# Optimization experiments

Measured on AMD Instinct MI355X. Metric: run time of the kernel, lower is better.

The kernel has to match this reference:

```python
import jax, jax.numpy as jnp
import numpy as np
import math

B, T, C = 4, 2048, 1024
H = 16
D_FF = 4 * C


def new_gelu(x):
    # tanh-approx GELU, identical to the torch.jit.script version
    return 0.5 * x * (1.0 + jnp.tanh(math.sqrt(2.0 / math.pi) * (x + 0.044715 * x ** 3)))


def layernorm(x, g, b, eps=1e-5):
    mu = jnp.mean(x, axis=-1, keepdims=True)
    var = jnp.var(x, axis=-1, keepdims=True)
    return (x - mu) * jax.lax.rsqrt(var + eps) * g + b


def setup_inputs() -> dict:
    key = jax.random.key(0)
    ks = jax.random.split(key, 8)
    s = 0.02
    return {
        "x": jax.random.normal(ks[0], (B, T, C), dtype=jnp.float32),
        "ln1_g": jnp.ones((C,), jnp.float32),
        "ln1_b": jnp.zeros((C,), jnp.float32),
        "w_qkv": jax.random.normal(ks[1], (C, 3 * C), jnp.float32) * s,
        "b_qkv": jnp.zeros((3 * C,), jnp.float32),
        "w_attnproj": jax.random.normal(ks[2], (C, C), jnp.float32) * s,
        "b_attnproj": jnp.zeros((C,), jnp.float32),
        "ln2_g": jnp.ones((C,), jnp.float32),
        "ln2_b": jnp.zeros((C,), jnp.float32),
        "w_fc": jax.random.normal(ks[3], (C, D_FF), jnp.float32) * s,
        "b_fc": jnp.zeros((D_FF,), jnp.float32),
        "w_proj": jax.random.normal(ks[4], (D_FF, C), jnp.float32) * s,
        "b_proj": jnp.zeros((C,), jnp.float32),
    }


def _block(x, ln1_g, ln1_b, w_qkv, b_qkv, w_attnproj, b_attnproj,
           ln2_g, ln2_b, w_fc, b_fc, w_proj, b_proj):
    # --- self-attention (pre-LN, non-causal, dropout=0) ---
    h = layernorm(x, ln1_g, ln1_b)
    qkv = h @ w_qkv + b_qkv                       # [B,T,3C]
    q, k, v = jnp.split(qkv, 3, axis=-1)
    hd = C // H
    q = q.reshape(B, T, H, hd).transpose(0, 2, 1, 3)  # [B,H,T,hd]
    k = k.reshape(B, T, H, hd).transpose(0, 2, 1, 3)
    v = v.reshape(B, T, H, hd).transpose(0, 2, 1, 3)
    att = jnp.einsum('bhqd,bhkd->bhqk', q, k) * (1.0 / math.sqrt(hd))
    att = jax.nn.softmax(att, axis=-1)
    y = jnp.einsum('bhqk,bhkd->bhqd', att, v)
    y = y.transpose(0, 2, 1, 3).reshape(B, T, C)
    x = x + (y @ w_attnproj + b_attnproj)
    # --- MLP ---
    h = layernorm(x, ln2_g, ln2_b)
    h = new_gelu(h @ w_fc + b_fc)
    x = x + (h @ w_proj + b_proj)
    return x


def reference(x, ln1_g, ln1_b, w_qkv, b_qkv, w_attnproj, b_attnproj,
              ln2_g, ln2_b, w_fc, b_fc, w_proj, b_proj):
    return _block(x, ln1_g, ln1_b, w_qkv, b_qkv, w_attnproj, b_attnproj,
                  ln2_g, ln2_b, w_fc, b_fc, w_proj, b_proj)
```

## Files before the change

kernel.cpp:

```cpp
#include <hip/hip_runtime.h>


typedef __attribute__((ext_vector_type(8))) short short8;
typedef __attribute__((ext_vector_type(4))) float fx4;
typedef __attribute__((ext_vector_type(16))) float fx16;

__device__ __forceinline__ unsigned short f2bf(float f) {
    union { float f; unsigned u; } v; v.f = f;
    unsigned r = v.u + 0x7fffu + ((v.u >> 16) & 1u);
    return (unsigned short)(r >> 16);
}

__device__ __forceinline__ float fexp2(float x) {
#if __has_builtin(__builtin_amdgcn_exp2f)
    return __builtin_amdgcn_exp2f(x);
#else
    return __expf(x * 0.69314718055994531f);
#endif
}

__device__ __forceinline__ unsigned pack_trunc(float lo, float hi) {
    return __builtin_amdgcn_perm(__float_as_uint(hi), __float_as_uint(lo),
                                 0x07060302u);
}

__device__ __forceinline__ void ld_lds16(const void* g, void* l) {
    __builtin_amdgcn_global_load_lds(
        (const __attribute__((address_space(1))) unsigned int*)g,
        (__attribute__((address_space(3))) unsigned int*)l, 16, 0, 0);
}

__global__ __launch_bounds__(256) void transpose_all(
    const float* __restrict__ w0, unsigned short* __restrict__ o0,
    const float* __restrict__ w1, unsigned short* __restrict__ o1,
    const float* __restrict__ w2, unsigned short* __restrict__ o2,
    const float* __restrict__ w3, unsigned short* __restrict__ o3)
{
    __shared__ float tile[32][33];
    int b = blockIdx.x;
    const float* in; unsigned short* out; int R, Cn;
    if (b < 3072)      { in = w0; out = o0; R = 1024; Cn = 3072; }
    else if (b < 4096) { b -= 3072; in = w1; out = o1; R = 1024; Cn = 1024; }
    else if (b < 8192) { b -= 4096; in = w2; out = o2; R = 1024; Cn = 4096; }
    else               { b -= 8192; in = w3; out = o3; R = 4096; Cn = 1024; }
    int tilesX = Cn >> 5;
    int c0 = (b % tilesX) * 32, r0 = (b / tilesX) * 32;
    int tx = threadIdx.x, ty = threadIdx.y;
    for (int i = 0; i < 4; ++i)
        tile[ty + i * 8][tx] = in[(size_t)(r0 + ty + i * 8) * Cn + c0 + tx];
    __syncthreads();
    for (int i = 0; i < 4; ++i)
        out[(size_t)(c0 + ty + i * 8) * R + r0 + tx] = f2bf(tile[tx][ty + i * 8]);
}

__global__ __launch_bounds__(256) void layernorm_bf16(
    const float* __restrict__ x, const float* __restrict__ g,
    const float* __restrict__ bb, unsigned short* __restrict__ out)
{
    const int C = 1024;
    int row = blockIdx.x;
    const float* xr = x + (size_t)row * C;
    float4 v = ((const float4*)xr)[threadIdx.x];
    float s  = v.x + v.y + v.z + v.w;
    float ss = v.x * v.x + v.y * v.y + v.z * v.z + v.w * v.w;
    for (int off = 32; off >= 1; off >>= 1) {
        s  += __shfl_xor(s,  off);
        ss += __shfl_xor(ss, off);
    }
    __shared__ float sbuf[2][4];
    int wave = threadIdx.x >> 6;
    if ((threadIdx.x & 63) == 0) { sbuf[0][wave] = s; sbuf[1][wave] = ss; }
    __syncthreads();
    s  = sbuf[0][0] + sbuf[0][1] + sbuf[0][2] + sbuf[0][3];
    ss = sbuf[1][0] + sbuf[1][1] + sbuf[1][2] + sbuf[1][3];
    float mu   = s * (1.0f / C);
    float var  = ss * (1.0f / C) - mu * mu;
    float rstd = rsqrtf(var + 1e-5f);
    int i = threadIdx.x * 4;
    ushort4 o;
    o.x = f2bf((v.x - mu) * rstd * g[i + 0] + bb[i + 0]);
    o.y = f2bf((v.y - mu) * rstd * g[i + 1] + bb[i + 1]);
    o.z = f2bf((v.z - mu) * rstd * g[i + 2] + bb[i + 2]);
    o.w = f2bf((v.w - mu) * rstd * g[i + 3] + bb[i + 3]);
    ((ushort4*)(out + (size_t)row * C))[threadIdx.x] = o;
}

template <int EPI>
__global__ __launch_bounds__(256) void gemm_bt(
    const unsigned short* __restrict__ A, const unsigned short* __restrict__ Bt,
    const float* __restrict__ bias, const float* __restrict__ resid,
    void* __restrict__ out0, void* __restrict__ out1, void* __restrict__ out2,
    int M, int N, int K)
{
    __shared__ unsigned short As[128 * 64];
    __shared__ unsigned short Bs[128 * 64];
    const int bm = blockIdx.y * 128, bn = blockIdx.x * 128;
    const int t = threadIdx.x, wave = t >> 6, lane = t & 63;
    const int wm = (wave >> 1) * 64, wn = (wave & 1) * 64;
    const int l32 = lane & 31, half = lane >> 5;

    int goff[4], loff[4];
    #pragma unroll
    for (int c = 0; c < 4; ++c) {
        int idx = t + c * 256;
        int row = idx >> 3, ps = idx & 7;
        int p = (ps - row) & 7;
        goff[c] = row * K + p * 8;
        loff[c] = idx * 8;
    }
    int aoffs[2][4], boffs[2][4];
    #pragma unroll
    for (int i = 0; i < 2; ++i)
        #pragma unroll
        for (int s = 0; s < 4; ++s) {
            int ra = wm + i * 32 + l32;
            int rb = wn + i * 32 + l32;
            aoffs[i][s] = ra * 64 + (((s * 2 + half + ra) & 7) << 3);
            boffs[i][s] = rb * 64 + (((s * 2 + half + rb) & 7) << 3);
        }

    const unsigned short* Ab = A + (size_t)bm * K;
    const unsigned short* Bb = Bt + (size_t)bn * K;

    fx16 acc[2][2];
    #pragma unroll
    for (int mi = 0; mi < 2; ++mi)
        #pragma unroll
        for (int ni = 0; ni < 2; ++ni)
            acc[mi][ni] = 0.0f;

    for (int it = 0, nit = K >> 6; it < nit; ++it) {
        #pragma unroll
        for (int c = 0; c < 4; ++c) {
            ld_lds16(Ab + goff[c], &As[loff[c]]);
            ld_lds16(Bb + goff[c], &Bs[loff[c]]);
        }
        Ab += 64; Bb += 64;
        __syncthreads();
        #pragma unroll
        for (int s = 0; s < 4; ++s) {
            short8 a0 = *(const short8*)&As[aoffs[0][s]];
            short8 a1 = *(const short8*)&As[aoffs[1][s]];
            short8 b0 = *(const short8*)&Bs[boffs[0][s]];
            short8 b1 = *(const short8*)&Bs[boffs[1][s]];
            acc[0][0] = __builtin_amdgcn_mfma_f32_32x32x16_bf16(a0, b0, acc[0][0], 0, 0, 0);
            acc[0][1] = __builtin_amdgcn_mfma_f32_32x32x16_bf16(a0, b1, acc[0][1], 0, 0, 0);
            acc[1][0] = __builtin_amdgcn_mfma_f32_32x32x16_bf16(a1, b0, acc[1][0], 0, 0, 0);
            acc[1][1] = __builtin_amdgcn_mfma_f32_32x32x16_bf16(a1, b1, acc[1][1], 0, 0, 0);
        }
        __syncthreads();
    }

    #pragma unroll
    for (int mi = 0; mi < 2; ++mi) {
        #pragma unroll
        for (int ni = 0; ni < 2; ++ni) {
            int col = bn + wn + ni * 32 + l32;
            float bcol = bias[col];
            #pragma unroll
            for (int reg = 0; reg < 16; ++reg) {
                int row = bm + wm + mi * 32 + (reg & 3) + 8 * (reg >> 2) + 4 * half;
                float v = acc[mi][ni][reg] + bcol;
                if constexpr (EPI == 0) {
                    int sec = col >> 10, cc = col & 1023;
                    int head = cc >> 6, d = cc & 63;
                    int batch = row >> 11, tt = row & 2047;
                    size_t bh = (size_t)(batch * 16 + head);
                    if (sec == 0)
                        ((unsigned short*)out0)[(bh * 2048 + tt) * 64 + d] =
                            f2bf(v * 0.18033688011112042f);
                    else if (sec == 1)
                        ((unsigned short*)out1)[(bh * 2048 + tt) * 64 + d] = f2bf(v);
                    else
                        ((unsigned short*)out2)[(bh * 64 + d) * 2048 + tt] = f2bf(v);
                } else if constexpr (EPI == 1) {
                    ((float*)out0)[(size_t)row * N + col] =
                        resid[(size_t)row * N + col] + v;
                } else {
                    float u2 = 1.5957691216057308f * (v + 0.044715f * v * v * v);
                    float gl = v * __builtin_amdgcn_rcpf(1.0f + __expf(-u2));
                    ((unsigned short*)out0)[(size_t)row * N + col] = f2bf(gl);
                }
            }
        }
    }
}

__global__ __launch_bounds__(256, 3) void flash_attn(
    const unsigned short* __restrict__ Q, const unsigned short* __restrict__ Kk,
    const unsigned short* __restrict__ Vt, unsigned short* __restrict__ Y)
{
    __shared__ unsigned short Ks[64 * 64];
    __shared__ unsigned short Vs[64 * 64];
    __shared__ unsigned short Ps[4][16 * 72];
    const int bh = blockIdx.y;
    const int batch = bh >> 4, head = bh & 15;
    const int t = threadIdx.x, w = t >> 6, lane = t & 63;
    const int lq = lane >> 4, lr = lane & 15;
    const int q0 = blockIdx.x * 128 + w * 32;
    const size_t base = (size_t)bh * 2048 * 64;

    short8 qf[2][2];
    #pragma unroll
    for (int qt = 0; qt < 2; ++qt)
        #pragma unroll
        for (int c = 0; c < 2; ++c)
            qf[qt][c] = *(const short8*)
                &Q[base + (size_t)(q0 + qt * 16 + lr) * 64 + c * 32 + lq * 8];

    int kg[2], vg[2], lo[2];
    #pragma unroll
    for (int c2 = 0; c2 < 2; ++c2) {
        int idx = t + c2 * 256;
        int row = idx >> 3, ps = idx & 7;
        int p = (ps - row) & 7;
        kg[c2] = row * 64 + p * 8;
        vg[c2] = row * 2048 + p * 8;
        lo[c2] = idx * 8;
    }
    int kvo[4][2];
    #pragma unroll
    for (int i = 0; i < 4; ++i)
        #pragma unroll
        for (int c = 0; c < 2; ++c) {
            int row = i * 16 + lr;
            kvo[i][c] = row * 64 + (((c * 4 + lq + row) & 7) << 3);
        }
    const unsigned short* Kb = Kk + base;
    const unsigned short* Vb = Vt + base;

    short8 ones;
    #pragma unroll
    for (int i = 0; i < 8; ++i) ones[i] = (short)0x3F80;

    fx4 lacc[2];
    fx4 o[2][4];
    #pragma unroll
    for (int qt = 0; qt < 2; ++qt) {
        lacc[qt] = 0.0f;
        #pragma unroll
        for (int dn = 0; dn < 4; ++dn) o[qt][dn] = 0.0f;
    }

    for (int kt = 0; kt < 32; ++kt) {
        __syncthreads();
        #pragma unroll
        for (int c2 = 0; c2 < 2; ++c2) {
            ld_lds16(Kb + kg[c2], &Ks[lo[c2]]);
            ld_lds16(Vb + vg[c2], &Vs[lo[c2]]);
        }
        Kb += 64 * 64; Vb += 64;
        __syncthreads();

        short8 kf[4][2], vf[4][2];
        #pragma unroll
        for (int kn = 0; kn < 4; ++kn)
            #pragma unroll
            for (int c = 0; c < 2; ++c)
                kf[kn][c] = *(const short8*)&Ks[kvo[kn][c]];
        #pragma unroll
        for (int dn = 0; dn < 4; ++dn)
            #pragma unroll
            for (int c = 0; c < 2; ++c)
                vf[dn][c] = *(const short8*)&Vs[kvo[dn][c]];

        #pragma unroll
        for (int qt = 0; qt < 2; ++qt) {
            #pragma unroll
            for (int kn = 0; kn < 4; ++kn) {
                fx4 s = 0.0f;
                s = __builtin_amdgcn_mfma_f32_16x16x32_bf16(
                    kf[kn][0], qf[qt][0], s, 0, 0, 0);
                s = __builtin_amdgcn_mfma_f32_16x16x32_bf16(
                    kf[kn][1], qf[qt][1], s, 0, 0, 0);
                float p0 = fexp2(s[0]);
                float p1 = fexp2(s[1]);
                float p2 = fexp2(s[2]);
                float p3 = fexp2(s[3]);
                uint2 pk;
                pk.x = pack_trunc(p0, p1);
                pk.y = pack_trunc(p2, p3);
                *(uint2*)&Ps[w][lr * 72 + kn * 16 + lq * 4] = pk;
            }
            short8 pf0 = *(const short8*)&Ps[w][lr * 72 + lq * 8];
            short8 pf1 = *(const short8*)&Ps[w][lr * 72 + 32 + lq * 8];
            lacc[qt] = __builtin_amdgcn_mfma_f32_16x16x32_bf16(
                ones, pf0, lacc[qt], 0, 0, 0);
            lacc[qt] = __builtin_amdgcn_mfma_f32_16x16x32_bf16(
                ones, pf1, lacc[qt], 0, 0, 0);
            #pragma unroll
            for (int dn = 0; dn < 4; ++dn) {
                o[qt][dn] = __builtin_amdgcn_mfma_f32_16x16x32_bf16(
                    vf[dn][0], pf0, o[qt][dn], 0, 0, 0);
                o[qt][dn] = __builtin_amdgcn_mfma_f32_16x16x32_bf16(
                    vf[dn][1], pf1, o[qt][dn], 0, 0, 0);
            }
        }
    }

    #pragma unroll
    for (int qt = 0; qt < 2; ++qt) {
        float inv = __builtin_amdgcn_rcpf(lacc[qt][0]);
        int qg = q0 + qt * 16 + lr;
        #pragma unroll
        for (int dn = 0; dn < 4; ++dn) {
            ushort4 ov;
            ov.x = f2bf(o[qt][dn][0] * inv);
            ov.y = f2bf(o[qt][dn][1] * inv);
            ov.z = f2bf(o[qt][dn][2] * inv);
            ov.w = f2bf(o[qt][dn][3] * inv);
            *(ushort4*)&Y[((size_t)(batch * 2048 + qg)) * 1024 +
                          head * 64 + dn * 16 + lq * 4] = ov;
        }
    }
}

extern "C" void kernel_launch(void* const* d_in, const int* in_sizes, int n_in,
                              void* d_out, int out_size, void* d_ws, size_t ws_size,
                              hipStream_t stream)
{
    const float* x      = (const float*)d_in[0];
    const float* ln1_g  = (const float*)d_in[1];
    const float* ln1_b  = (const float*)d_in[2];
    const float* w_qkv  = (const float*)d_in[3];
    const float* b_qkv  = (const float*)d_in[4];
    const float* w_ap   = (const float*)d_in[5];
    const float* b_ap   = (const float*)d_in[6];
    const float* ln2_g  = (const float*)d_in[7];
    const float* ln2_b  = (const float*)d_in[8];
    const float* w_fc   = (const float*)d_in[9];
    const float* b_fc   = (const float*)d_in[10];
    const float* w_proj = (const float*)d_in[11];
    const float* b_proj = (const float*)d_in[12];
    float* out = (float*)d_out;

    char* ws = (char*)d_ws;
    unsigned short* wT_qkv = (unsigned short*)(ws + 0);
    unsigned short* wT_ap  = (unsigned short*)(ws + 6291456);
    unsigned short* wT_fc  = (unsigned short*)(ws + 8388608);
    unsigned short* wT_pr  = (unsigned short*)(ws + 16777216);
    float*          x2     = (float*)(ws + 25165824);
    unsigned short* Abuf   = (unsigned short*)(ws + 58720256);
    unsigned short* Qb     = (unsigned short*)(ws + 75497472);
    unsigned short* Kb     = (unsigned short*)(ws + 75497472 + 16777216);
    unsigned short* Vtb    = (unsigned short*)(ws + 75497472 + 33554432);
    unsigned short* H3     = (unsigned short*)(ws + 75497472);

    transpose_all<<<12288, dim3(32, 8), 0, stream>>>(
        w_qkv, wT_qkv, w_ap, wT_ap, w_fc, wT_fc, w_proj, wT_pr);

    layernorm_bf16<<<8192, 256, 0, stream>>>(x, ln1_g, ln1_b, Abuf);
    gemm_bt<0><<<dim3(24, 64), 256, 0, stream>>>(Abuf, wT_qkv, b_qkv, nullptr,
                                                 Qb, Kb, Vtb, 8192, 3072, 1024);
    flash_attn<<<dim3(16, 64), 256, 0, stream>>>(Qb, Kb, Vtb, Abuf);
    gemm_bt<1><<<dim3(8, 64), 256, 0, stream>>>(Abuf, wT_ap, b_ap, x,
                                                x2, nullptr, nullptr, 8192, 1024, 1024);
    layernorm_bf16<<<8192, 256, 0, stream>>>(x2, ln2_g, ln2_b, Abuf);
    gemm_bt<2><<<dim3(32, 64), 256, 0, stream>>>(Abuf, wT_fc, b_fc, nullptr,
                                                 H3, nullptr, nullptr, 8192, 4096, 1024);
    gemm_bt<1><<<dim3(8, 64), 256, 0, stream>>>(H3, wT_pr, b_proj, x2,
                                                out, nullptr, nullptr, 8192, 1024, 4096);
}
```

Baseline: 514.3 us.

## Double-buffer A tile in LDS and stream B fragments from global into registers

The bf16 GEMM now double-buffers the A tile in shared memory and prefetches the next K-slice while the current one is computed, with one barrier per stage instead of two. The B operand no longer goes through LDS: each wave loads its MFMA fragments straight from global memory into double-buffered registers. The aim is to hide load latency behind MFMA work and to halve LDS traffic and footprint. In exchange, waves that share the same columns load the same B data twice from global memory or cache, the B accesses are strided and less coalesced, and the register-held fragments raise register pressure.

After: 699.9 us. +36.1%, slower.

```diff
diff --git a/kernel.cpp b/kernel.cpp
--- a/kernel.cpp
+++ b/kernel.cpp
@@ -92,8 +92,7 @@
     void* __restrict__ out0, void* __restrict__ out1, void* __restrict__ out2,
     int M, int N, int K)
 {
-    __shared__ unsigned short As[128 * 64];
-    __shared__ unsigned short Bs[128 * 64];
+    __shared__ unsigned short As[2][128 * 64];
     const int bm = blockIdx.y * 128, bn = blockIdx.x * 128;
     const int t = threadIdx.x, wave = t >> 6, lane = t & 63;
     const int wm = (wave >> 1) * 64, wn = (wave & 1) * 64;
@@ -108,16 +107,20 @@
         goff[c] = row * K + p * 8;
         loff[c] = idx * 8;
     }
-    int aoffs[2][4], boffs[2][4];
+    int aoffs[2][4];
     #pragma unroll
     for (int i = 0; i < 2; ++i)
         #pragma unroll
         for (int s = 0; s < 4; ++s) {
             int ra = wm + i * 32 + l32;
-            int rb = wn + i * 32 + l32;
             aoffs[i][s] = ra * 64 + (((s * 2 + half + ra) & 7) << 3);
-            boffs[i][s] = rb * 64 + (((s * 2 + half + rb) & 7) << 3);
-        }
+        }
+    int bgo[2][4];
+    #pragma unroll
+    for (int i = 0; i < 2; ++i)
+        #pragma unroll
+        for (int s = 0; s < 4; ++s)
+            bgo[i][s] = (wn + i * 32 + l32) * K + s * 16 + half * 8;
 
     const unsigned short* Ab = A + (size_t)bm * K;
     const unsigned short* Bb = Bt + (size_t)bn * K;
@@ -129,26 +132,43 @@
         for (int ni = 0; ni < 2; ++ni)
             acc[mi][ni] = 0.0f;
 
-    for (int it = 0, nit = K >> 6; it < nit; ++it) {
-        #pragma unroll
-        for (int c = 0; c < 4; ++c) {
-            ld_lds16(Ab + goff[c], &As[loff[c]]);
-            ld_lds16(Bb + goff[c], &Bs[loff[c]]);
-        }
+    short8 bcur[2][4], bnxt[2][4];
+
+    auto prefetch = [&](int buf, short8 (&bf)[2][4]) {
+        #pragma unroll
+        for (int c = 0; c < 4; ++c)
+            ld_lds16(Ab + goff[c], &As[buf][loff[c]]);
+        #pragma unroll
+        for (int i = 0; i < 2; ++i)
+            #pragma unroll
+            for (int s = 0; s < 4; ++s)
+                bf[i][s] = *(const short8*)(Bb + bgo[i][s]);
         Ab += 64; Bb += 64;
+    };
+    auto compute = [&](int buf, short8 (&bf)[2][4]) {
+        #pragma unroll
+        for (int s = 0; s < 4; ++s) {
+            short8 a0 = *(const short8*)&As[buf][aoffs[0][s]];
+            short8 a1 = *(const short8*)&As[buf][aoffs[1][s]];
+            acc[0][0] = __builtin_amdgcn_mfma_f32_32x32x16_bf16(a0, bf[0][s], acc[0][0], 0, 0, 0);
+            acc[0][1] = __builtin_amdgcn_mfma_f32_32x32x16_bf16(a0, bf[1][s], acc[0][1], 0, 0, 0);
+            acc[1][0] = __builtin_amdgcn_mfma_f32_32x32x16_bf16(a1, bf[0][s], acc[1][0], 0, 0, 0);
+            acc[1][1] = __builtin_amdgcn_mfma_f32_32x32x16_bf16(a1, bf[1][s], acc[1][1], 0, 0, 0);
+        }
+    };
+
+    const int nit = K >> 6;
+    prefetch(0, bcur);
+    __syncthreads();
+    for (int it = 0; it < nit; it += 2) {
+        if (it + 1 < nit) prefetch(1, bnxt);
+        compute(0, bcur);
         __syncthreads();
-        #pragma unroll
-        for (int s = 0; s < 4; ++s) {
-            short8 a0 = *(const short8*)&As[aoffs[0][s]];
-            short8 a1 = *(const short8*)&As[aoffs[1][s]];
-            short8 b0 = *(const short8*)&Bs[boffs[0][s]];
-            short8 b1 = *(const short8*)&Bs[boffs[1][s]];
-            acc[0][0] = __builtin_amdgcn_mfma_f32_32x32x16_bf16(a0, b0, acc[0][0], 0, 0, 0);
-            acc[0][1] = __builtin_amdgcn_mfma_f32_32x32x16_bf16(a0, b1, acc[0][1], 0, 0, 0);
-            acc[1][0] = __builtin_amdgcn_mfma_f32_32x32x16_bf16(a1, b0, acc[1][0], 0, 0, 0);
-            acc[1][1] = __builtin_amdgcn_mfma_f32_32x32x16_bf16(a1, b1, acc[1][1], 0, 0, 0);
-        }
-        __syncthreads();
+        if (it + 1 < nit) {
+            if (it + 2 < nit) prefetch(0, bcur);
+            compute(1, bnxt);
+            __syncthreads();
+        }
     }
 
     #pragma unroll
```
